# Optimization experiments

Measured on AMD Instinct MI355X. Metric: run time of the kernel, lower is better.

Reference implementation:

```python
import jax, jax.numpy as jnp
import numpy as np

TOTAL = 2097152      # total rows (sum of sizes)
N_SEG = 4096         # number of segments
W = 3                # windowSize from init
FEAT = 64


def _make_sizes(key):
    # random partition of TOTAL into N_SEG parts, each >= W
    rem = TOTAL - N_SEG * W
    cuts = jnp.sort(jax.random.randint(key, (N_SEG - 1,), 0, rem + 1))
    bounds = jnp.concatenate([jnp.zeros(1, jnp.int64 if cuts.dtype == jnp.int64 else jnp.int32), cuts, jnp.full((1,), rem, cuts.dtype)])
    return (jnp.diff(bounds) + W).astype(jnp.int32)


def setup_inputs() -> dict:
    key = jax.random.key(0)
    k1, k2 = jax.random.split(key)
    input = jax.random.normal(k1, (TOTAL, FEAT), dtype=jnp.float32)
    sizes = _make_sizes(k2)
    return {"input": input, "sizes": sizes}


def reference(input, sizes):
    # Segmented max over ragged rows: segment i covers rows
    # [start_i, start_i + sizes[i] - W + 1); the last W-1 rows of each
    # segment are excluded from the reduction (as in the torch loop).
    n = sizes.shape[0]
    ends = jnp.cumsum(sizes)                       # [n]
    starts = ends - sizes                          # [n]
    rows = jnp.arange(input.shape[0])              # [total]
    seg = jnp.searchsorted(ends, rows, side='right')  # segment id per row
    offset = rows - starts[seg]
    valid = offset < (sizes[seg] - W + 1)
    ids = jnp.where(valid, seg, n)                 # dump invalid rows in bin n
    out = jax.ops.segment_max(input, ids, num_segments=n + 1)
    return out[:n]                                 # [n, feat]
```

## Files before the change

kernel.cpp:

```cpp
#include <hip/hip_runtime.h>
#include <math.h>

#define TOTAL 2097152
#define N_SEG 4096
#define FEAT 64
#define WINDOW 3
#define ROWS_PER_BLOCK 512
#define N_CHUNK (TOTAL / ROWS_PER_BLOCK)
#define INIT_BLOCKS (N_SEG * FEAT / 4 / 256)

__global__ __launch_bounds__(256) void dmax_setup_kernel(
    const int* __restrict__ sizes, int* __restrict__ starts,
    float* __restrict__ out) {
  const int b = blockIdx.x;
  const int t = threadIdx.x;

  if (b < INIT_BLOCKS) {
    const int i = b * 256 + t;
    reinterpret_cast<float4*>(out)[i] =
        make_float4(-INFINITY, -INFINITY, -INFINITY, -INFINITY);
    return;
  }

  if (t >= 64) return;
  const int per = N_SEG / 64;
  const int base = t * per;

  int s = 0;
#pragma unroll 4
  for (int i = 0; i < per; ++i) s += sizes[base + i];

  int v = s;
#pragma unroll
  for (int d = 1; d < 64; d <<= 1) {
    int o = __shfl_up(v, d, 64);
    if (t >= d) v += o;
  }
  int run = v - s;

  for (int i = 0; i < per; ++i) {
    starts[base + i] = run;
    run += sizes[base + i];
  }
}

__global__ __launch_bounds__(256) void dmax_chunk_kernel(
    const float* __restrict__ in, const int* __restrict__ sizes,
    const int* __restrict__ starts, float* __restrict__ out) {
  const int chunk_lo = blockIdx.x * ROWS_PER_BLOCK;
  const int chunk_hi = chunk_lo + ROWS_PER_BLOCK;

  const int t = threadIdx.x;
  const int fchunk = t & 15;
  const int rowslot = t >> 4;
  const int wave = t >> 6;

  int lo = 0, hi = N_SEG - 1;
  while (lo < hi) {
    int mid = (lo + hi + 1) >> 1;
    if (starts[mid] <= chunk_lo) lo = mid; else hi = mid - 1;
  }
  int seg = lo;

  __shared__ float red[4][FEAT];
  const float* basep = in + fchunk * 4;

  int row = chunk_lo;
  while (row < chunk_hi) {
    const int s_start = starts[seg];
    const int s_size = sizes[seg];
    const int s_vend = s_start + s_size - (WINDOW - 1);
    const int s_end = s_start + s_size;

    const int rlo = row;
    const int rhi = min(chunk_hi, s_vend);

    if (rhi > rlo) {
      float4 m = make_float4(-INFINITY, -INFINITY, -INFINITY, -INFINITY);
#pragma unroll 8
      for (int r = rlo + rowslot; r < rhi; r += 16) {
        const float4 v =
            *reinterpret_cast<const float4*>(basep + (size_t)r * FEAT);
        m.x = fmaxf(m.x, v.x);
        m.y = fmaxf(m.y, v.y);
        m.z = fmaxf(m.z, v.z);
        m.w = fmaxf(m.w, v.w);
      }
#pragma unroll
      for (int mask = 16; mask <= 32; mask <<= 1) {
        m.x = fmaxf(m.x, __shfl_xor(m.x, mask, 64));
        m.y = fmaxf(m.y, __shfl_xor(m.y, mask, 64));
        m.z = fmaxf(m.z, __shfl_xor(m.z, mask, 64));
        m.w = fmaxf(m.w, __shfl_xor(m.w, mask, 64));
      }
      __syncthreads();
      if ((t & 63) < 16) {
        red[wave][fchunk * 4 + 0] = m.x;
        red[wave][fchunk * 4 + 1] = m.y;
        red[wave][fchunk * 4 + 2] = m.z;
        red[wave][fchunk * 4 + 3] = m.w;
      }
      __syncthreads();
      if (t < FEAT) {
        float v = fmaxf(fmaxf(red[0][t], red[1][t]),
                        fmaxf(red[2][t], red[3][t]));
        unsafeAtomicMax(out + (size_t)seg * FEAT + t, v);
      }
    }

    row = min(chunk_hi, s_end);
    ++seg;
  }
}

extern "C" void kernel_launch(void* const* d_in, const int* in_sizes, int n_in,
                              void* d_out, int out_size, void* d_ws, size_t ws_size,
                              hipStream_t stream) {
  const float* input = (const float*)d_in[0];
  const int* sizes = (const int*)d_in[1];
  float* out = (float*)d_out;
  int* starts = (int*)d_ws;

  dmax_setup_kernel<<<INIT_BLOCKS + 1, 256, 0, stream>>>(sizes, starts, out);
  dmax_chunk_kernel<<<N_CHUNK, 256, 0, stream>>>(input, sizes, starts, out);
}
```

Baseline: 112.9 us.

## Use nontemporal 8-row-per-thread loads, larger chunks, and block-wide parallel prefix in setup

Doubles rows per block and restructures the streaming loop so each thread loads 8 consecutive rows per iteration with nontemporal loads, using two accumulators and a masked tail. The setup kernel now stages sizes in shared memory and computes the prefix sum across all 256 threads with a cross-wave combine instead of one wave doing serial loops. The aim is more memory-level parallelism and less cache pollution on a bandwidth-bound scan, plus a shorter serial setup. Larger chunks mean fewer blocks and more segment-boundary iterations per block.

```diff
diff --git a/kernel.cpp b/kernel.cpp
--- a/kernel.cpp
+++ b/kernel.cpp
@@ -5,9 +5,24 @@
 #define N_SEG 4096
 #define FEAT 64
 #define WINDOW 3
-#define ROWS_PER_BLOCK 512
+#define ROWS_PER_BLOCK 1024
 #define N_CHUNK (TOTAL / ROWS_PER_BLOCK)
 #define INIT_BLOCKS (N_SEG * FEAT / 4 / 256)
+
+typedef float f32x4 __attribute__((ext_vector_type(4)));
+
+__device__ __forceinline__ f32x4 nt_load(const f32x4* p) {
+  return __builtin_nontemporal_load(p);
+}
+
+__device__ __forceinline__ f32x4 vmax4(f32x4 a, f32x4 b) {
+  f32x4 r;
+  r.x = fmaxf(a.x, b.x);
+  r.y = fmaxf(a.y, b.y);
+  r.z = fmaxf(a.z, b.z);
+  r.w = fmaxf(a.w, b.w);
+  return r;
+}
 
 __global__ __launch_bounds__(256) void dmax_setup_kernel(
     const int* __restrict__ sizes, int* __restrict__ starts,
@@ -17,30 +32,43 @@
 
   if (b < INIT_BLOCKS) {
     const int i = b * 256 + t;
-    reinterpret_cast<float4*>(out)[i] =
-        make_float4(-INFINITY, -INFINITY, -INFINITY, -INFINITY);
+    f32x4 v = {-INFINITY, -INFINITY, -INFINITY, -INFINITY};
+    reinterpret_cast<f32x4*>(out)[i] = v;
     return;
   }
 
-  if (t >= 64) return;
-  const int per = N_SEG / 64;
-  const int base = t * per;
+  __shared__ int s_sz[N_SEG];
+#pragma unroll
+  for (int i = 0; i < N_SEG / 256; ++i) s_sz[t + i * 256] = sizes[t + i * 256];
+  __syncthreads();
+
+  const int lane = t & 63;
+  const int wave = t >> 6;
 
   int s = 0;
-#pragma unroll 4
-  for (int i = 0; i < per; ++i) s += sizes[base + i];
+#pragma unroll
+  for (int i = 0; i < 16; ++i) s += s_sz[t * 16 + i];
 
   int v = s;
 #pragma unroll
   for (int d = 1; d < 64; d <<= 1) {
     int o = __shfl_up(v, d, 64);
-    if (t >= d) v += o;
+    if (lane >= d) v += o;
   }
-  int run = v - s;
 
-  for (int i = 0; i < per; ++i) {
-    starts[base + i] = run;
-    run += sizes[base + i];
+  __shared__ int wtot[4];
+  if (lane == 63) wtot[wave] = v;
+  __syncthreads();
+
+  int wpre = 0;
+  for (int w = 0; w < 4; ++w)
+    if (w < wave) wpre += wtot[w];
+
+  int run = wpre + v - s;
+#pragma unroll
+  for (int i = 0; i < 16; ++i) {
+    starts[t * 16 + i] = run;
+    run += s_sz[t * 16 + i];
   }
 }
 
@@ -63,7 +91,7 @@
   int seg = lo;
 
   __shared__ float red[4][FEAT];
-  const float* basep = in + fchunk * 4;
+  const f32x4* inv = reinterpret_cast<const f32x4*>(in);
 
   int row = chunk_lo;
   while (row < chunk_hi) {
@@ -76,16 +104,36 @@
     const int rhi = min(chunk_hi, s_vend);
 
     if (rhi > rlo) {
-      float4 m = make_float4(-INFINITY, -INFINITY, -INFINITY, -INFINITY);
-#pragma unroll 8
-      for (int r = rlo + rowslot; r < rhi; r += 16) {
-        const float4 v =
-            *reinterpret_cast<const float4*>(basep + (size_t)r * FEAT);
-        m.x = fmaxf(m.x, v.x);
-        m.y = fmaxf(m.y, v.y);
-        m.z = fmaxf(m.z, v.z);
-        m.w = fmaxf(m.w, v.w);
+      f32x4 m0 = {-INFINITY, -INFINITY, -INFINITY, -INFINITY};
+      f32x4 m1 = m0;
+
+      int rb = rlo + rowslot * 8;
+      const f32x4* p = inv + (size_t)rb * (FEAT / 4) + fchunk;
+
+      for (; rb + 8 <= rhi; rb += 128, p += 128 * (FEAT / 4)) {
+        f32x4 v0 = nt_load(p + 0 * 16);
+        f32x4 v1 = nt_load(p + 1 * 16);
+        f32x4 v2 = nt_load(p + 2 * 16);
+        f32x4 v3 = nt_load(p + 3 * 16);
+        f32x4 v4 = nt_load(p + 4 * 16);
+        f32x4 v5 = nt_load(p + 5 * 16);
+        f32x4 v6 = nt_load(p + 6 * 16);
+        f32x4 v7 = nt_load(p + 7 * 16);
+        m0 = vmax4(m0, vmax4(vmax4(v0, v1), vmax4(v2, v3)));
+        m1 = vmax4(m1, vmax4(vmax4(v4, v5), vmax4(v6, v7)));
       }
+      if (rb < rhi) {
+        const int nrem = rhi - rb;
+#pragma unroll
+        for (int k = 0; k < 7; ++k) {
+          if (k < nrem) {
+            f32x4 v = nt_load(p + k * 16);
+            m0 = vmax4(m0, v);
+          }
+        }
+      }
+      f32x4 m = vmax4(m0, m1);
+
 #pragma unroll
       for (int mask = 16; mask <= 32; mask <<= 1) {
         m.x = fmaxf(m.x, __shfl_xor(m.x, mask, 64));
```

Result: faster. 104.9 us (-7.0%).
